# Kernel tuning notes

Hardware: AMD Instinct MI355X
Metric: run time of the kernel (lower is better)

Reference implementation:

```python
import jax, jax.numpy as jnp
import numpy as np
import math

EMBED_DIM = 768
HEADS = 6
HEAD_DIM = EMBED_DIM // HEADS


def setup_inputs() -> dict:
    key = jax.random.key(0)
    ks = jax.random.split(key, 9)
    B, L, D = 4, 2048, EMBED_DIM
    s = 1.0 / math.sqrt(D)
    return {
        "x_input": jax.random.normal(ks[0], (B, L, D), dtype=jnp.float32),
        "Wq": jax.random.normal(ks[1], (D, D), dtype=jnp.float32) * s,
        "bq": jnp.zeros((D,), dtype=jnp.float32),
        "Wk": jax.random.normal(ks[2], (D, D), dtype=jnp.float32) * s,
        "bk": jnp.zeros((D,), dtype=jnp.float32),
        "Wv": jax.random.normal(ks[3], (D, D), dtype=jnp.float32) * s,
        "bv": jnp.zeros((D,), dtype=jnp.float32),
        "Wo": jax.random.normal(ks[4], (D, D), dtype=jnp.float32) * s,
        "bo": jnp.zeros((D,), dtype=jnp.float32),
    }


def reference(x_input, Wq, bq, Wk, bk, Wv, bv, Wo, bo):
    B, L, D = x_input.shape
    # QKV projections
    q = x_input @ Wq + bq
    k = x_input @ Wk + bk
    v = x_input @ Wv + bv
    # [B, L, D] -> [B, H, L, hd]
    def split_heads(t):
        return t.reshape(B, L, HEADS, HEAD_DIM).transpose(0, 2, 1, 3)
    q, k, v = split_heads(q), split_heads(k), split_heads(v)
    # scaled dot-product scores [B, H, L, L]
    scores = jnp.einsum("bhqd,bhkd->bhqk", q, k) / math.sqrt(HEAD_DIM)
    # causal mask: query i attends to keys j <= i
    causal = jnp.tril(jnp.ones((L, L), dtype=bool))
    scores = jnp.where(causal, scores, jnp.finfo(scores.dtype).min)
    attn = jax.nn.softmax(scores, axis=-1)
    out = jnp.einsum("bhqk,bhkd->bhqd", attn, v)  # [B, H, L, hd]
    out = out.transpose(0, 2, 1, 3).reshape(B, L, D)
    # output projection (dropout = identity in eval mode)
    return out @ Wo + bo
```

## Files before the change

kernel.cpp:

```cpp
#include <hip/hip_runtime.h>
#include <hip/hip_bf16.h>
#include <stdint.h>

#define D_EMB 768
#define NHEADS 6
#define HD 128
#define BATCH 4
#define SEQ 2048
#define BH (BATCH*NHEADS)
#define M_ROWS (BATCH*SEQ)

typedef float f32x4 __attribute__((ext_vector_type(4)));
typedef __bf16 bf16x8 __attribute__((ext_vector_type(8)));
typedef short short8 __attribute__((ext_vector_type(8)));

__device__ __forceinline__ short f2bf(float f) {
  union { float f; uint32_t u; } x; x.f = f;
  uint32_t r = x.u + 0x7fffu + ((x.u >> 16) & 1u);
  return (short)(r >> 16);
}

__device__ __forceinline__ void gload16(const void* g, void* l) {
  __builtin_amdgcn_global_load_lds(
      (const __attribute__((address_space(1))) unsigned int*)g,
      (__attribute__((address_space(3))) unsigned int*)l, 16, 0, 0);
}

__global__ void cvt_f32_bf16_k(const float* __restrict__ in, short* __restrict__ out, int n4) {
  int i = blockIdx.x * 256 + threadIdx.x;
  if (i >= n4) return;
  float4 v = ((const float4*)in)[i];
  short4 o;
  o.x = f2bf(v.x); o.y = f2bf(v.y); o.z = f2bf(v.z); o.w = f2bf(v.w);
  ((short4*)out)[i] = o;
}

__global__ void transpose_w_k(const float* __restrict__ in, short* __restrict__ out, int R, int C) {
  __shared__ float tile[32][33];
  int c0 = blockIdx.x * 32, r0 = blockIdx.y * 32;
  int tx = threadIdx.x, ty = threadIdx.y;
  #pragma unroll
  for (int i = 0; i < 32; i += 8)
    tile[ty + i][tx] = in[(size_t)(r0 + ty + i) * C + (c0 + tx)];
  __syncthreads();
  #pragma unroll
  for (int i = 0; i < 32; i += 8)
    out[(size_t)(c0 + ty + i) * R + (r0 + tx)] = f2bf(tile[tx][ty + i]);
}

__global__ void transpose_v_k(const short* __restrict__ in, short* __restrict__ out) {
  __shared__ short tile[32][33];
  const int hidx = blockIdx.z;
  const short* src = in + (size_t)hidx * SEQ * HD;
  short* dst = out + (size_t)hidx * SEQ * HD;
  int d0 = blockIdx.x * 32;
  int l0 = blockIdx.y * 32;
  int tx = threadIdx.x, ty = threadIdx.y;
  #pragma unroll
  for (int i = 0; i < 32; i += 8)
    tile[ty + i][tx] = src[(size_t)(l0 + ty + i) * HD + d0 + tx];
  __syncthreads();
  #pragma unroll
  for (int i = 0; i < 32; i += 8)
    dst[(size_t)(d0 + ty + i) * SEQ + l0 + tx] = tile[tx][ty + i];
}

__global__ __launch_bounds__(256) void gemm_bt_k(
    const short* __restrict__ A, const short* __restrict__ BT,
    const float* __restrict__ b0, const float* __restrict__ b1, const float* __restrict__ b2,
    float* __restrict__ Cf, short* __restrict__ Cb,
    int M, int N, int K, int mode)
{
  __shared__ short Als[2][128 * 32];
  __shared__ short Bls[2][128 * 32];
  const int tid = threadIdx.x;
  const int lane = tid & 63;
  const int wave = tid >> 6;
  const int m0 = blockIdx.x * 128;
  const int n0 = blockIdx.y * 128;
  const int wm = (wave & 1) * 64;
  const int wn = (wave >> 1) * 64;
  const int frow = lane & 15;
  const int kk = (lane >> 4) * 8;

  #define G_STAGE(buf, k0)                                                       \
    do {                                                                         \
      _Pragma("unroll")                                                          \
      for (int i = 0; i < 2; ++i) {                                              \
        gload16(&A[(size_t)(m0 + i * 64 + (tid >> 2)) * K + (k0) + (tid & 3) * 8], \
                (char*)Als[buf] + i * 4096 + wave * 1024);                       \
        gload16(&BT[(size_t)(n0 + i * 64 + (tid >> 2)) * K + (k0) + (tid & 3) * 8], \
                (char*)Bls[buf] + i * 4096 + wave * 1024);                       \
      }                                                                          \
    } while (0)

  f32x4 acc[4][4] = {};
  G_STAGE(0, 0);
  __syncthreads();
  int buf = 0;
  for (int k0 = 0; k0 < K; k0 += 32) {
    if (k0 + 32 < K) G_STAGE(buf ^ 1, k0 + 32);
    bf16x8 af[4], bfv[4];
    #pragma unroll
    for (int i = 0; i < 4; ++i) {
      af[i]  = *(const bf16x8*)((const char*)Als[buf] + (wm + i * 16 + frow) * 64 + kk * 2);
      bfv[i] = *(const bf16x8*)((const char*)Bls[buf] + (wn + i * 16 + frow) * 64 + kk * 2);
    }
    #pragma unroll
    for (int i = 0; i < 4; ++i)
      #pragma unroll
      for (int j = 0; j < 4; ++j)
        acc[i][j] = __builtin_amdgcn_mfma_f32_16x16x32_bf16(af[i], bfv[j], acc[i][j], 0, 0, 0);
    __syncthreads();
    buf ^= 1;
  }
  #undef G_STAGE

  const int r0l = (lane >> 4) * 4;
  const int cl = lane & 15;
  const int t3 = n0 / 768;
  const int nloc = n0 - t3 * 768;
  const float* bp = (t3 == 0) ? b0 : ((t3 == 1) ? b1 : b2);
  short* Cbt = Cb + (size_t)t3 * ((size_t)BH * SEQ * HD);
  #pragma unroll
  for (int i = 0; i < 4; ++i) {
    #pragma unroll
    for (int j = 0; j < 4; ++j) {
      int coll = nloc + wn + j * 16 + cl;
      float bv = bp[coll];
      #pragma unroll
      for (int r = 0; r < 4; ++r) {
        int m = m0 + wm + i * 16 + r0l + r;
        float v = acc[i][j][r] + bv;
        if (mode == 0) {
          Cf[(size_t)m * N + (n0 + wn + j * 16 + cl)] = v;
        } else {
          int b = m >> 11, li = m & 2047;
          int h = coll >> 7, d = coll & 127;
          Cbt[((((size_t)b * NHEADS + h) << 11) + li) * HD + d] = f2bf(v);
        }
      }
    }
  }
}

__global__ __launch_bounds__(256, 2) void attn_causal_k(
    const short* __restrict__ Q, const short* __restrict__ K,
    const short* __restrict__ Vt, short* __restrict__ O)
{
  __shared__ __attribute__((aligned(16))) short Kls[2][64 * 128];
  __shared__ __attribute__((aligned(16))) short Vls[2][128 * 64];
  __shared__ __attribute__((aligned(16))) short Pls[4][16 * 64];

  const int tid = threadIdx.x;
  const int lane = tid & 63;
  const int wave = tid >> 6;
  const int g = lane >> 4;
  const int cl = lane & 15;

  const int bid = (int)blockIdx.x;
  const int sid = (bid & 7) * 96 + (bid >> 3);
  const int bh = sid >> 5;
  const int qb = 31 - (sid & 31);
  const int q0 = qb * 64;
  const int qw0 = q0 + wave * 16;

  const short* Qh = Q + (size_t)bh * SEQ * HD;
  const short* Kh = K + (size_t)bh * SEQ * HD;
  const short* Vh = Vt + (size_t)bh * SEQ * HD;

  bf16x8 qf[4];
  #pragma unroll
  for (int c = 0; c < 4; ++c)
    qf[c] = *(const bf16x8*)&Qh[(size_t)(qw0 + cl) * HD + c * 32 + g * 8];

  f32x4 o[8] = {};
  float lrow[4] = {0.f, 0.f, 0.f, 0.f};

  const float kSc = 0.08838834764831845f * 1.44269504088896341f;
  const int swzr = (cl & 7) << 4;
  char* Pw = (char*)&Pls[wave][0];
  const int nt = qb + 1;

  #define STAGE(b, t)                                                            \
    do {                                                                         \
      const int j0s = (t) * 64;                                                  \
      _Pragma("unroll")                                                          \
      for (int i = 0; i < 4; ++i) {                  \
        int row = i * 16 + wave * 4 + (lane >> 4);                               \
        int colb = ((lane & 15) * 16) ^ ((row & 7) << 4);                        \
        gload16((const char*)Kh + (size_t)(j0s + row) * 256 + colb,              \
                (char*)Kls[b] + i * 4096 + wave * 1024);                         \
      }                                                                          \
      _Pragma("unroll")                                                          \
      for (int i = 0; i < 4; ++i) {                 \
        int row = i * 32 + wave * 8 + (lane >> 3);                               \
        int colb = ((lane & 7) * 16) ^ ((row & 7) << 4);                         \
        gload16((const char*)Vh + ((size_t)row * SEQ + j0s) * 2 + colb,          \
                (char*)Vls[b] + i * 4096 + wave * 1024);                         \
      }                                                                          \
    } while (0)

  STAGE(0, 0);
  int buf = 0;
  for (int t = 0; t < nt; ++t) {
    __syncthreads();
    if (t + 1 < nt) STAGE(buf ^ 1, t + 1);
    const int j0 = t * 64;

    f32x4 s[4] = {};
    #pragma unroll
    for (int jf = 0; jf < 4; ++jf)
      #pragma unroll
      for (int c = 0; c < 4; ++c) {
        bf16x8 kf = *(const bf16x8*)((const char*)Kls[buf] + (jf * 16 + cl) * 256 +
                                     ((c * 64 + g * 16) ^ swzr));
        s[jf] = __builtin_amdgcn_mfma_f32_16x16x32_bf16(qf[c], kf, s[jf], 0, 0, 0);
      }

    #pragma unroll
    for (int r = 0; r < 4; ++r) {
      const int qi = qw0 + g * 4 + r;
      const int rl = g * 4 + r;
      const int swzw = (rl & 7) << 4;
      float ps = 0.f;
      #pragma unroll
      for (int jf = 0; jf < 4; ++jf) {
        const int j = j0 + jf * 16 + cl;
        float p = (j > qi) ? 0.f : __builtin_amdgcn_exp2f(s[jf][r] * kSc);
        ps += p;
        *(short*)(Pw + rl * 128 + (((jf * 16 + cl) * 2) ^ swzw)) = f2bf(p);
      }
      lrow[r] += ps;
    }
    asm volatile("s_waitcnt lgkmcnt(0)" ::: "memory");
    __builtin_amdgcn_sched_barrier(0);

    #pragma unroll
    for (int ks = 0; ks < 2; ++ks) {
      bf16x8 pf = *(const bf16x8*)(Pw + cl * 128 + ((ks * 64 + g * 16) ^ swzr));
      #pragma unroll
      for (int f = 0; f < 8; ++f) {
        bf16x8 vf = *(const bf16x8*)((const char*)Vls[buf] + (f * 16 + cl) * 128 +
                                     ((ks * 64 + g * 16) ^ swzr));
        o[f] = __builtin_amdgcn_mfma_f32_16x16x32_bf16(pf, vf, o[f], 0, 0, 0);
      }
    }
    buf ^= 1;
  }
  #undef STAGE

  #pragma unroll
  for (int r = 0; r < 4; ++r)
    #pragma unroll
    for (int off2 = 1; off2 < 16; off2 <<= 1)
      lrow[r] += __shfl_xor(lrow[r], off2);

  const int b = bh / NHEADS, h = bh % NHEADS;
  #pragma unroll
  for (int r = 0; r < 4; ++r) {
    const int qi = qw0 + g * 4 + r;
    const float invl = 1.0f / lrow[r];
    size_t base = ((size_t)b * SEQ + qi) * D_EMB + h * HD;
    #pragma unroll
    for (int f = 0; f < 8; ++f)
      O[base + f * 16 + cl] = f2bf(o[f][r] * invl);
  }
}

extern "C" void kernel_launch(void* const* d_in, const int* in_sizes, int n_in,
                              void* d_out, int out_size, void* d_ws, size_t ws_size,
                              hipStream_t stream) {
  const float* x  = (const float*)d_in[0];
  const float* Wq = (const float*)d_in[1];
  const float* bq = (const float*)d_in[2];
  const float* Wk = (const float*)d_in[3];
  const float* bk = (const float*)d_in[4];
  const float* Wv = (const float*)d_in[5];
  const float* bv = (const float*)d_in[6];
  const float* Wo = (const float*)d_in[7];
  const float* bo = (const float*)d_in[8];
  float* out = (float*)d_out;

  char* ws = (char*)d_ws;
  size_t off = 0;
  auto carve = [&](size_t bytes) {
    char* p = ws + off;
    off += (bytes + 255) & ~(size_t)255;
    return p;
  };
  short* xb     = (short*)carve((size_t)M_ROWS * D_EMB * 2);
  short* wqkvT  = (short*)carve((size_t)3 * D_EMB * D_EMB * 2);
  short* wot    = (short*)carve((size_t)D_EMB * D_EMB * 2);
  short* Qb  = (short*)carve((size_t)BH * SEQ * HD * 2);
  short* Kb  = (short*)carve((size_t)BH * SEQ * HD * 2);
  short* Vb  = (short*)carve((size_t)BH * SEQ * HD * 2);
  short* Vtb = (short*)carve((size_t)BH * SEQ * HD * 2);
  short* Ob  = (short*)carve((size_t)M_ROWS * D_EMB * 2);
  (void)Kb; (void)Vb;

  int n4 = M_ROWS * D_EMB / 4;
  cvt_f32_bf16_k<<<(n4 + 255) / 256, 256, 0, stream>>>(x, xb, n4);

  dim3 tb(32, 8);
  transpose_w_k<<<dim3(24, 24), tb, 0, stream>>>(Wq, wqkvT,                 D_EMB, D_EMB);
  transpose_w_k<<<dim3(24, 24), tb, 0, stream>>>(Wk, wqkvT +     D_EMB*D_EMB, D_EMB, D_EMB);
  transpose_w_k<<<dim3(24, 24), tb, 0, stream>>>(Wv, wqkvT + 2 * D_EMB*D_EMB, D_EMB, D_EMB);
  transpose_w_k<<<dim3(24, 24), tb, 0, stream>>>(Wo, wot, D_EMB, D_EMB);

  gemm_bt_k<<<dim3(M_ROWS / 128, (3 * D_EMB) / 128), 256, 0, stream>>>(
      xb, wqkvT, bq, bk, bv, nullptr, Qb, M_ROWS, 3 * D_EMB, D_EMB, 1);

  transpose_v_k<<<dim3(HD / 32, SEQ / 32, BH), tb, 0, stream>>>(Vb, Vtb);

  attn_causal_k<<<dim3(768), 256, 0, stream>>>(Qb, Kb, Vtb, Ob);

  gemm_bt_k<<<dim3(M_ROWS / 128, D_EMB / 128), 256, 0, stream>>>(
      Ob, wot, bo, bo, bo, out, nullptr, M_ROWS, D_EMB, D_EMB, 0);
}
```

Measured before the change: 239.2 us.

## Fuse V transpose into QKV GEMM epilogue and permute key order in attention

The QKV GEMM epilogue now writes the V slice straight into the transposed [BH, HD, SEQ] layout, using packed 4-element bf16 stores. This removes the separate transpose_v_k launch and its round trip through memory. In attention, each lane now owns keys 4*cl+jf instead of jf*16+cl, with a matching change to the K LDS swizzle, so the four P values per row can be packed into one 8-byte LDS store instead of four 2-byte stores. The MFMA phases are also wrapped in s_setprio to favour matrix issue. The risks are strided global stores in the V epilogue and a changed swizzle that could add LDS bank conflicts.

Measured after the change: 233.5 us. 2.4% less time.

```diff
diff --git a/kernel.cpp b/kernel.cpp
--- a/kernel.cpp
+++ b/kernel.cpp
@@ -19,6 +19,9 @@
   uint32_t r = x.u + 0x7fffu + ((x.u >> 16) & 1u);
   return (short)(r >> 16);
 }
+__device__ __forceinline__ uint32_t f2bf_pk(float lo, float hi) {
+  return (uint32_t)(uint16_t)f2bf(lo) | ((uint32_t)(uint16_t)f2bf(hi) << 16);
+}
 
 __device__ __forceinline__ void gload16(const void* g, void* l) {
   __builtin_amdgcn_global_load_lds(
@@ -48,27 +51,10 @@
     out[(size_t)(c0 + ty + i) * R + (r0 + tx)] = f2bf(tile[tx][ty + i]);
 }
 
-__global__ void transpose_v_k(const short* __restrict__ in, short* __restrict__ out) {
-  __shared__ short tile[32][33];
-  const int hidx = blockIdx.z;
-  const short* src = in + (size_t)hidx * SEQ * HD;
-  short* dst = out + (size_t)hidx * SEQ * HD;
-  int d0 = blockIdx.x * 32;
-  int l0 = blockIdx.y * 32;
-  int tx = threadIdx.x, ty = threadIdx.y;
-  #pragma unroll
-  for (int i = 0; i < 32; i += 8)
-    tile[ty + i][tx] = src[(size_t)(l0 + ty + i) * HD + d0 + tx];
-  __syncthreads();
-  #pragma unroll
-  for (int i = 0; i < 32; i += 8)
-    dst[(size_t)(d0 + ty + i) * SEQ + l0 + tx] = tile[tx][ty + i];
-}
-
 __global__ __launch_bounds__(256) void gemm_bt_k(
     const short* __restrict__ A, const short* __restrict__ BT,
     const float* __restrict__ b0, const float* __restrict__ b1, const float* __restrict__ b2,
-    float* __restrict__ Cf, short* __restrict__ Cb,
+    float* __restrict__ Cf, short* __restrict__ Cb, short* __restrict__ Vt,
     int M, int N, int K, int mode)
 {
   __shared__ short Als[2][128 * 32];
@@ -128,16 +114,27 @@
     for (int j = 0; j < 4; ++j) {
       int coll = nloc + wn + j * 16 + cl;
       float bv = bp[coll];
-      #pragma unroll
-      for (int r = 0; r < 4; ++r) {
-        int m = m0 + wm + i * 16 + r0l + r;
-        float v = acc[i][j][r] + bv;
-        if (mode == 0) {
-          Cf[(size_t)m * N + (n0 + wn + j * 16 + cl)] = v;
-        } else {
+      if (mode == 0) {
+        #pragma unroll
+        for (int r = 0; r < 4; ++r) {
+          int m = m0 + wm + i * 16 + r0l + r;
+          Cf[(size_t)m * N + (n0 + wn + j * 16 + cl)] = acc[i][j][r] + bv;
+        }
+      } else if (t3 == 2) {
+        int mb = m0 + wm + i * 16 + r0l;
+        int b = mb >> 11, li = mb & 2047;
+        int h = coll >> 7, d = coll & 127;
+        uint2 w;
+        w.x = f2bf_pk(acc[i][j][0] + bv, acc[i][j][1] + bv);
+        w.y = f2bf_pk(acc[i][j][2] + bv, acc[i][j][3] + bv);
+        *(uint2*)&Vt[(((size_t)b * NHEADS + h) * HD + d) * SEQ + li] = w;
+      } else {
+        #pragma unroll
+        for (int r = 0; r < 4; ++r) {
+          int m = m0 + wm + i * 16 + r0l + r;
           int b = m >> 11, li = m & 2047;
           int h = coll >> 7, d = coll & 127;
-          Cbt[((((size_t)b * NHEADS + h) << 11) + li) * HD + d] = f2bf(v);
+          Cbt[((((size_t)b * NHEADS + h) << 11) + li) * HD + d] = f2bf(acc[i][j][r] + bv);
         }
       }
     }
@@ -188,7 +185,7 @@
       _Pragma("unroll")                                                          \
       for (int i = 0; i < 4; ++i) {                  \
         int row = i * 16 + wave * 4 + (lane >> 4);                               \
-        int colb = ((lane & 15) * 16) ^ ((row & 7) << 4);                        \
+        int colb = ((lane & 15) * 16) ^ (((row >> 2) & 7) << 4);                 \
         gload16((const char*)Kh + (size_t)(j0s + row) * 256 + colb,              \
                 (char*)Kls[b] + i * 4096 + wave * 1024);                         \
       }                                                                          \
@@ -209,33 +206,39 @@
     const int j0 = t * 64;
 
     f32x4 s[4] = {};
-    #pragma unroll
-    for (int jf = 0; jf < 4; ++jf)
+    __builtin_amdgcn_s_setprio(1);
+    #pragma unroll
+    for (int jf = 0; jf < 4; ++jf) {
+      const int key = 4 * cl + jf;
       #pragma unroll
       for (int c = 0; c < 4; ++c) {
-        bf16x8 kf = *(const bf16x8*)((const char*)Kls[buf] + (jf * 16 + cl) * 256 +
-                                     ((c * 64 + g * 16) ^ swzr));
+        bf16x8 kf = *(const bf16x8*)((const char*)Kls[buf] + key * 256 +
+                                     ((c * 64 + g * 16) ^ (((key >> 2) & 7) << 4)));
         s[jf] = __builtin_amdgcn_mfma_f32_16x16x32_bf16(qf[c], kf, s[jf], 0, 0, 0);
       }
+    }
+    __builtin_amdgcn_s_setprio(0);
 
     #pragma unroll
     for (int r = 0; r < 4; ++r) {
       const int qi = qw0 + g * 4 + r;
       const int rl = g * 4 + r;
-      const int swzw = (rl & 7) << 4;
-      float ps = 0.f;
+      float p[4];
       #pragma unroll
       for (int jf = 0; jf < 4; ++jf) {
-        const int j = j0 + jf * 16 + cl;
-        float p = (j > qi) ? 0.f : __builtin_amdgcn_exp2f(s[jf][r] * kSc);
-        ps += p;
-        *(short*)(Pw + rl * 128 + (((jf * 16 + cl) * 2) ^ swzw)) = f2bf(p);
+        const int j = j0 + 4 * cl + jf;
+        p[jf] = (j > qi) ? 0.f : __builtin_amdgcn_exp2f(s[jf][r] * kSc);
       }
-      lrow[r] += ps;
+      lrow[r] += (p[0] + p[1]) + (p[2] + p[3]);
+      uint2 w;
+      w.x = f2bf_pk(p[0], p[1]);
+      w.y = f2bf_pk(p[2], p[3]);
+      *(uint2*)(Pw + rl * 128 + ((cl * 8) ^ ((rl & 7) << 4))) = w;
     }
     asm volatile("s_waitcnt lgkmcnt(0)" ::: "memory");
     __builtin_amdgcn_sched_barrier(0);
 
+    __builtin_amdgcn_s_setprio(1);
     #pragma unroll
     for (int ks = 0; ks < 2; ++ks) {
       bf16x8 pf = *(const bf16x8*)(Pw + cl * 128 + ((ks * 64 + g * 16) ^ swzr));
@@ -246,6 +249,7 @@
         o[f] = __builtin_amdgcn_mfma_f32_16x16x32_bf16(pf, vf, o[f], 0, 0, 0);
       }
     }
+    __builtin_amdgcn_s_setprio(0);
     buf ^= 1;
   }
   #undef STAGE
@@ -294,27 +298,23 @@
   short* wot    = (short*)carve((size_t)D_EMB * D_EMB * 2);
   short* Qb  = (short*)carve((size_t)BH * SEQ * HD * 2);
   short* Kb  = (short*)carve((size_t)BH * SEQ * HD * 2);
-  short* Vb  = (short*)carve((size_t)BH * SEQ * HD * 2);
   short* Vtb = (short*)carve((size_t)BH * SEQ * HD * 2);
   short* Ob  = (short*)carve((size_t)M_ROWS * D_EMB * 2);
-  (void)Kb; (void)Vb;
 
   int n4 = M_ROWS * D_EMB / 4;
   cvt_f32_bf16_k<<<(n4 + 255) / 256, 256, 0, stream>>>(x, xb, n4);
 
   dim3 tb(32, 8);
-  transpose_w_k<<<dim3(24, 24), tb, 0, stream>>>(Wq, wqkvT,                 D_EMB, D_EMB);
+  transpose_w_k<<<dim3(24, 24), tb, 0, stream>>>(Wq, wqkvT,                   D_EMB, D_EMB);
   transpose_w_k<<<dim3(24, 24), tb, 0, stream>>>(Wk, wqkvT +     D_EMB*D_EMB, D_EMB, D_EMB);
   transpose_w_k<<<dim3(24, 24), tb, 0, stream>>>(Wv, wqkvT + 2 * D_EMB*D_EMB, D_EMB, D_EMB);
   transpose_w_k<<<dim3(24, 24), tb, 0, stream>>>(Wo, wot, D_EMB, D_EMB);
 
   gemm_bt_k<<<dim3(M_ROWS / 128, (3 * D_EMB) / 128), 256, 0, stream>>>(
-      xb, wqkvT, bq, bk, bv, nullptr, Qb, M_ROWS, 3 * D_EMB, D_EMB, 1);
-
-  transpose_v_k<<<dim3(HD / 32, SEQ / 32, BH), tb, 0, stream>>>(Vb, Vtb);
+      xb, wqkvT, bq, bk, bv, nullptr, Qb, Vtb, M_ROWS, 3 * D_EMB, D_EMB, 1);
 
   attn_causal_k<<<dim3(768), 256, 0, stream>>>(Qb, Kb, Vtb, Ob);
 
   gemm_bt_k<<<dim3(M_ROWS / 128, D_EMB / 128), 256, 0, stream>>>(
-      Ob, wot, bo, bo, bo, out, nullptr, M_ROWS, D_EMB, D_EMB, 0);
-}
+      Ob, wot, bo, bo, bo, out, nullptr, nullptr, M_ROWS, D_EMB, D_EMB, 0);
+}
```
